# Kernel optimization log

Measured on AMD Instinct MI355X. Metric: run time of the kernel, lower is better.

The kernel has to match this reference:

```python
import jax, jax.numpy as jnp
import numpy as np

B, S, D, H = 4, 2048, 1024, 16
HD = D // H  # head_dim = 64


def setup_inputs() -> dict:
    key = jax.random.key(0)
    ks = jax.random.split(key, 11)
    scale = 1.0 / np.sqrt(D)
    return {
        "query": jax.random.normal(ks[0], (B, S, D), jnp.float32),
        "key": jax.random.normal(ks[1], (B, S, D), jnp.float32),
        "value": jax.random.normal(ks[2], (B, S, D), jnp.float32),
        "Wq": jax.random.normal(ks[3], (D, D), jnp.float32) * scale,
        "bq": jnp.zeros((D,), jnp.float32),
        "Wk": jax.random.normal(ks[4], (D, D), jnp.float32) * scale,
        "bk": jnp.zeros((D,), jnp.float32),
        "Wv": jax.random.normal(ks[5], (D, D), jnp.float32) * scale,
        "bv": jnp.zeros((D,), jnp.float32),
        "Wo": jax.random.normal(ks[6], (D, D), jnp.float32) * scale,
        "bo": jnp.zeros((D,), jnp.float32),
    }


def _split_heads(x):
    # [B, S, D] -> [B, H, S, HD]
    return x.reshape(B, -1, H, HD).transpose(0, 2, 1, 3)


def reference(query, key, value, Wq, bq, Wk, bk, Wv, bv, Wo, bo):
    # QKV projections in fp32, then cast to fp16 (faithful to the torch code)
    q = (query @ Wq.T + bq).astype(jnp.float16)
    k = (key @ Wk.T + bk).astype(jnp.float16)
    v = (value @ Wv.T + bv).astype(jnp.float16)
    q, k, v = _split_heads(q), _split_heads(k), _split_heads(v)
    # scores in fp16, scaled by sqrt(head_dim)
    energy = jnp.einsum("bhqd,bhkd->bhqk", q, k) / jnp.float16(np.sqrt(HD))
    attention = jax.nn.softmax(energy, axis=-1)  # fp16 softmax, as in torch
    x = jnp.einsum("bhqk,bhkd->bhqd", attention, v).astype(jnp.float32)
    x = x.transpose(0, 2, 1, 3).reshape(B, -1, D)  # merge heads
    return x @ Wo.T + bo
```

## Files before the change

### kernel.cpp

```cpp
#include <hip/hip_runtime.h>
#include <cstdint>

#define BB 4
#define SS 2048
#define DD 1024
#define HH 16
#define HDIM 64
#define MTOT (BB*SS)

using half_t = _Float16;
typedef _Float16 half2v __attribute__((ext_vector_type(2)));
typedef _Float16 half4v __attribute__((ext_vector_type(4)));
typedef _Float16 half8v __attribute__((ext_vector_type(8)));
typedef float f32x4 __attribute__((ext_vector_type(4)));

#if defined(__has_builtin)
#if __has_builtin(__builtin_amdgcn_exp2f)
#define ATTN_EXP2(x) __builtin_amdgcn_exp2f(x)
#endif
#if __has_builtin(__builtin_amdgcn_cvt_pkrtz)
#define ATTN_PKRTZ 1
#endif
#endif

__device__ __forceinline__ void glds16(const half_t* g, half_t* l) {
    __builtin_amdgcn_global_load_lds(g, l, 16, 0, 0);
}

__global__ __launch_bounds__(256) void split_hi_lo(const float* __restrict__ x,
    half_t* __restrict__ hi, half_t* __restrict__ lo, int n4)
{
    const int i = blockIdx.x * blockDim.x + threadIdx.x;
    if (i >= n4) return;
    float4 v = reinterpret_cast<const float4*>(x)[i];
    float vv[4] = {v.x, v.y, v.z, v.w};
    half4v h, l;
    #pragma unroll
    for (int j = 0; j < 4; ++j) {
        half_t hh = (half_t)vv[j];
        h[j] = hh;
        l[j] = (half_t)(vv[j] - (float)hh);
    }
    reinterpret_cast<half4v*>(hi)[i] = h;
    reinterpret_cast<half4v*>(lo)[i] = l;
}

__global__ __launch_bounds__(256) void cast_w4(
    const float* __restrict__ w0, const float* __restrict__ w1,
    const float* __restrict__ w2, const float* __restrict__ w3,
    half_t* __restrict__ hi)
{
    const int z = blockIdx.z;
    const float* src = z == 0 ? w0 : z == 1 ? w1 : z == 2 ? w2 : w3;
    const size_t base4 = (size_t)z * (DD * DD / 4);
    const size_t i = base4 + blockIdx.x * 256 + threadIdx.x;
    float4 v = reinterpret_cast<const float4*>(src)[blockIdx.x * 256 + threadIdx.x];
    float vv[4] = {v.x, v.y, v.z, v.w};
    half4v h;
    #pragma unroll
    for (int j = 0; j < 4; ++j) h[j] = (half_t)vv[j];
    reinterpret_cast<half4v*>(hi)[i] = h;
}

__global__ __launch_bounds__(256, 4) void gemm_proj(
    const float* __restrict__ A0, const float* __restrict__ A1,
    const float* __restrict__ A2,
    const half_t* __restrict__ WH,
    const float* __restrict__ B0, const float* __restrict__ B1,
    const float* __restrict__ B2,
    half_t* __restrict__ C0, half_t* __restrict__ C1, half_t* __restrict__ C2)
{
    __shared__ __align__(16) half_t AhS[2][128 * 32];
    __shared__ __align__(16) half_t WhS[2][128 * 32];

    const int z = blockIdx.z;
    const float*  A    = z == 0 ? A0 : z == 1 ? A1 : A2;
    const float*  bias = z == 0 ? B0 : z == 1 ? B1 : B2;
    half_t*       C    = z == 0 ? C0 : z == 1 ? C1 : C2;
    const half_t* WHz  = WH + (size_t)z * (DD * DD);

    const int tid = threadIdx.x;
    const int l = tid & 63, w = tid >> 6;
    const int lr = l & 15, lg = l >> 4;
    const int wr = w >> 1, wc = w & 1;
    const int m0 = blockIdx.x * 128, n0 = blockIdx.y * 128;

    const int arow = tid >> 2;
    const int acol = (tid & 3) * 8;
    const int wlrow = l >> 2, wlcol = (l & 3) * 8;

    f32x4 acc[4][4] = {};
    float4 av[2][2];

    #pragma unroll
    for (int j = 0; j < 2; ++j) {
        const float* ap = A + (size_t)(m0 + j * 64 + arow) * DD + acol;
        av[j][0] = *reinterpret_cast<const float4*>(ap);
        av[j][1] = *reinterpret_cast<const float4*>(ap + 4);
    }
    #pragma unroll
    for (int j = 0; j < 2; ++j) {
        half_t hb[8];
        float v0[4] = {av[j][0].x, av[j][0].y, av[j][0].z, av[j][0].w};
        float v1[4] = {av[j][1].x, av[j][1].y, av[j][1].z, av[j][1].w};
        #pragma unroll
        for (int e = 0; e < 4; ++e) { hb[e] = (half_t)v0[e]; hb[4 + e] = (half_t)v1[e]; }
        *reinterpret_cast<int4*>(&AhS[0][(j * 64 + arow) * 32 + acol]) = *reinterpret_cast<int4*>(hb);
    }
    #pragma unroll
    for (int i = 0; i < 2; ++i) {
        const int rr = (w * 2 + i) * 16 + wlrow;
        glds16(WHz + (size_t)(n0 + rr) * DD + wlcol, &WhS[0][(w * 2 + i) * 512]);
    }
    #pragma unroll
    for (int j = 0; j < 2; ++j) {
        const float* ap = A + (size_t)(m0 + j * 64 + arow) * DD + 32 + acol;
        av[j][0] = *reinterpret_cast<const float4*>(ap);
        av[j][1] = *reinterpret_cast<const float4*>(ap + 4);
    }
    __syncthreads();

    for (int t = 0; t < 32; ++t) {
        const int cur = t & 1, nxt = cur ^ 1;
        if (t < 31) {
            const int kk1 = (t + 1) * 32;
            #pragma unroll
            for (int i = 0; i < 2; ++i) {
                const int rr = (w * 2 + i) * 16 + wlrow;
                glds16(WHz + (size_t)(n0 + rr) * DD + kk1 + wlcol, &WhS[nxt][(w * 2 + i) * 512]);
            }
            #pragma unroll
            for (int j = 0; j < 2; ++j) {
                half_t hb[8];
                float v0[4] = {av[j][0].x, av[j][0].y, av[j][0].z, av[j][0].w};
                float v1[4] = {av[j][1].x, av[j][1].y, av[j][1].z, av[j][1].w};
                #pragma unroll
                for (int e = 0; e < 4; ++e) { hb[e] = (half_t)v0[e]; hb[4 + e] = (half_t)v1[e]; }
                *reinterpret_cast<int4*>(&AhS[nxt][(j * 64 + arow) * 32 + acol]) = *reinterpret_cast<int4*>(hb);
            }
        }

        half8v af[4];
        #pragma unroll
        for (int mt = 0; mt < 4; ++mt)
            af[mt] = *reinterpret_cast<const half8v*>(&AhS[cur][(wr * 64 + mt * 16 + lr) * 32 + 8 * lg]);
        #pragma unroll
        for (int nt = 0; nt < 4; ++nt) {
            half8v wf = *reinterpret_cast<const half8v*>(&WhS[cur][(wc * 64 + nt * 16 + lr) * 32 + 8 * lg]);
            #pragma unroll
            for (int mt = 0; mt < 4; ++mt)
                acc[mt][nt] = __builtin_amdgcn_mfma_f32_16x16x32_f16(af[mt], wf, acc[mt][nt], 0, 0, 0);
        }

        if (t < 30) {
            const int kk2 = (t + 2) * 32;
            #pragma unroll
            for (int j = 0; j < 2; ++j) {
                const float* ap = A + (size_t)(m0 + j * 64 + arow) * DD + kk2 + acol;
                av[j][0] = *reinterpret_cast<const float4*>(ap);
                av[j][1] = *reinterpret_cast<const float4*>(ap + 4);
            }
        }
        __syncthreads();
    }

    #pragma unroll
    for (int nt = 0; nt < 4; ++nt) {
        const int n = n0 + wc * 64 + nt * 16 + lr;
        const float bn = bias[n];
        #pragma unroll
        for (int mt = 0; mt < 4; ++mt) {
            const int mbase = m0 + wr * 64 + mt * 16 + 4 * lg;
            #pragma unroll
            for (int j = 0; j < 4; ++j)
                C[(size_t)(mbase + j) * DD + n] = (half_t)(acc[mt][nt][j] + bn);
        }
    }
}

__global__ __launch_bounds__(256, 4) void gemm_out(
    const half_t* __restrict__ Ag,
    const half_t* __restrict__ WHz,
    const float* __restrict__ bias, float* __restrict__ C)
{
    __shared__ __align__(16) half_t AhS[2][128 * 32];
    __shared__ __align__(16) half_t WhS[2][128 * 32];

    const int tid = threadIdx.x;
    const int l = tid & 63, w = tid >> 6;
    const int lr = l & 15, lg = l >> 4;
    const int wr = w >> 1, wc = w & 1;
    const int m0 = blockIdx.x * 128, n0 = blockIdx.y * 128;
    const int wlrow = l >> 2, wlcol = (l & 3) * 8;

    f32x4 acc[4][4] = {};

    #pragma unroll
    for (int i = 0; i < 2; ++i) {
        const int rr = (w * 2 + i) * 16 + wlrow;
        glds16(Ag  + (size_t)(m0 + rr) * DD + wlcol, &AhS[0][(w * 2 + i) * 512]);
        glds16(WHz + (size_t)(n0 + rr) * DD + wlcol, &WhS[0][(w * 2 + i) * 512]);
    }
    __syncthreads();

    for (int t = 0; t < 32; ++t) {
        const int cur = t & 1, nxt = cur ^ 1;
        if (t < 31) {
            const int kk1 = (t + 1) * 32;
            #pragma unroll
            for (int i = 0; i < 2; ++i) {
                const int rr = (w * 2 + i) * 16 + wlrow;
                glds16(Ag  + (size_t)(m0 + rr) * DD + kk1 + wlcol, &AhS[nxt][(w * 2 + i) * 512]);
                glds16(WHz + (size_t)(n0 + rr) * DD + kk1 + wlcol, &WhS[nxt][(w * 2 + i) * 512]);
            }
        }

        half8v af[4];
        #pragma unroll
        for (int mt = 0; mt < 4; ++mt)
            af[mt] = *reinterpret_cast<const half8v*>(&AhS[cur][(wr * 64 + mt * 16 + lr) * 32 + 8 * lg]);
        #pragma unroll
        for (int nt = 0; nt < 4; ++nt) {
            half8v wf = *reinterpret_cast<const half8v*>(&WhS[cur][(wc * 64 + nt * 16 + lr) * 32 + 8 * lg]);
            #pragma unroll
            for (int mt = 0; mt < 4; ++mt)
                acc[mt][nt] = __builtin_amdgcn_mfma_f32_16x16x32_f16(af[mt], wf, acc[mt][nt], 0, 0, 0);
        }
        __syncthreads();
    }

    #pragma unroll
    for (int nt = 0; nt < 4; ++nt) {
        const int n = n0 + wc * 64 + nt * 16 + lr;
        const float bn = bias[n];
        #pragma unroll
        for (int mt = 0; mt < 4; ++mt) {
            const int mbase = m0 + wr * 64 + mt * 16 + 4 * lg;
            #pragma unroll
            for (int j = 0; j < 4; ++j)
                C[(size_t)(mbase + j) * DD + n] = acc[mt][nt][j] + bn;
        }
    }
}

template<int MODE, typename TC>
__global__ __launch_bounds__(256) void gemm3s(
    const half_t* __restrict__ Ah, const half_t* __restrict__ Al,
    const float* __restrict__ Af,
    const half_t* __restrict__ Wh, const half_t* __restrict__ Wl,
    const float* __restrict__ bias, TC* __restrict__ C,
    int Kdim, int Ndim)
{
    constexpr int LDT = 72;
    __shared__ __align__(16) half_t As[128 * LDT];
    __shared__ __align__(16) half_t Ws[128 * LDT];
    const int tid = threadIdx.x;
    const int l = tid & 63, w = tid >> 6;
    const int lr = l & 15, lg = l >> 4;
    const int wr = w >> 1, wc = w & 1;
    const int m0 = blockIdx.y * 128, n0 = blockIdx.x * 128;
    const int r = tid >> 1, t = tid & 1;

    f32x4 acc[4][4] = {};

    for (int kk = 0; kk < Kdim; kk += 32) {
        __syncthreads();
        if constexpr (MODE == 1) {
            const float* ap = Af + (size_t)(m0 + r) * Kdim + kk + 16 * t;
            half_t hbuf[16], lbuf[16];
            #pragma unroll
            for (int u = 0; u < 4; ++u) {
                float4 v = *reinterpret_cast<const float4*>(ap + 4 * u);
                float vv[4] = {v.x, v.y, v.z, v.w};
                #pragma unroll
                for (int j = 0; j < 4; ++j) {
                    half_t hh = (half_t)vv[j];
                    hbuf[4 * u + j] = hh;
                    lbuf[4 * u + j] = (half_t)(vv[j] - (float)hh);
                }
            }
            *reinterpret_cast<int4*>(&As[r * LDT + 16 * t])          = *reinterpret_cast<int4*>(hbuf);
            *reinterpret_cast<int4*>(&As[r * LDT + 16 * t + 8])      = *reinterpret_cast<int4*>(hbuf + 8);
            *reinterpret_cast<int4*>(&As[r * LDT + 40 + 16 * t])     = *reinterpret_cast<int4*>(lbuf);
            *reinterpret_cast<int4*>(&As[r * LDT + 40 + 16 * t + 8]) = *reinterpret_cast<int4*>(lbuf + 8);
        } else {
            const half_t* ap = Ah + (size_t)(m0 + r) * Kdim + kk + 16 * t;
            *reinterpret_cast<int4*>(&As[r * LDT + 16 * t])     = *reinterpret_cast<const int4*>(ap);
            *reinterpret_cast<int4*>(&As[r * LDT + 16 * t + 8]) = *reinterpret_cast<const int4*>(ap + 8);
        }
        {
            const half_t* wp = Wh + (size_t)(n0 + r) * Kdim + kk + 16 * t;
            *reinterpret_cast<int4*>(&Ws[r * LDT + 16 * t])     = *reinterpret_cast<const int4*>(wp);
            *reinterpret_cast<int4*>(&Ws[r * LDT + 16 * t + 8]) = *reinterpret_cast<const int4*>(wp + 8);
            const half_t* wlp = Wl + (size_t)(n0 + r) * Kdim + kk + 16 * t;
            *reinterpret_cast<int4*>(&Ws[r * LDT + 40 + 16 * t])     = *reinterpret_cast<const int4*>(wlp);
            *reinterpret_cast<int4*>(&Ws[r * LDT + 40 + 16 * t + 8]) = *reinterpret_cast<const int4*>(wlp + 8);
        }
        __syncthreads();

        half8v af[4], alf[4];
        #pragma unroll
        for (int mt = 0; mt < 4; ++mt) {
            af[mt] = *reinterpret_cast<const half8v*>(&As[(wr * 64 + mt * 16 + lr) * LDT + 8 * lg]);
            if constexpr (MODE != 2)
                alf[mt] = *reinterpret_cast<const half8v*>(&As[(wr * 64 + mt * 16 + lr) * LDT + 40 + 8 * lg]);
        }
        #pragma unroll
        for (int nt = 0; nt < 4; ++nt) {
            half8v wf  = *reinterpret_cast<const half8v*>(&Ws[(wc * 64 + nt * 16 + lr) * LDT + 8 * lg]);
            half8v wlf = *reinterpret_cast<const half8v*>(&Ws[(wc * 64 + nt * 16 + lr) * LDT + 40 + 8 * lg]);
            #pragma unroll
            for (int mt = 0; mt < 4; ++mt) {
                acc[mt][nt] = __builtin_amdgcn_mfma_f32_16x16x32_f16(af[mt], wf, acc[mt][nt], 0, 0, 0);
                acc[mt][nt] = __builtin_amdgcn_mfma_f32_16x16x32_f16(af[mt], wlf, acc[mt][nt], 0, 0, 0);
                if constexpr (MODE != 2)
                    acc[mt][nt] = __builtin_amdgcn_mfma_f32_16x16x32_f16(alf[mt], wf, acc[mt][nt], 0, 0, 0);
            }
        }
    }

    #pragma unroll
    for (int nt = 0; nt < 4; ++nt) {
        const int n = n0 + wc * 64 + nt * 16 + lr;
        const float bn = bias[n];
        #pragma unroll
        for (int mt = 0; mt < 4; ++mt) {
            const int mbase = m0 + wr * 64 + mt * 16 + 4 * lg;
            #pragma unroll
            for (int j = 0; j < 4; ++j) {
                float v = acc[mt][nt][j] + bn;
                if constexpr (sizeof(TC) == 4)
                    C[(size_t)(mbase + j) * Ndim + n] = v;
                else
                    C[(size_t)(mbase + j) * Ndim + n] = (half_t)v;
            }
        }
    }
}

template<typename TA, typename TC>
__global__ __launch_bounds__(256) void gemm_bias(const TA* __restrict__ A,
    const float* __restrict__ W, const float* __restrict__ bias,
    TC* __restrict__ C, int Mdim, int Ndim, int Kdim)
{
    constexpr int BK = 16;
    __shared__ float As[BK][68];
    __shared__ float Ws[BK][68];
    const int tx = threadIdx.x, ty = threadIdx.y;
    const int tid = ty * 16 + tx;
    const int m0 = blockIdx.y * 64, n0 = blockIdx.x * 64;
    const int lrow = tid >> 2;
    const int lc4  = (tid & 3) * 4;

    float acc[4][4] = {};
    for (int kk = 0; kk < Kdim; kk += BK) {
        {
            const TA* ap = A + (size_t)(m0 + lrow) * Kdim + kk + lc4;
            float a0, a1, a2, a3;
            if constexpr (sizeof(TA) == 4) {
                float4 v = *reinterpret_cast<const float4*>(ap);
                a0 = v.x; a1 = v.y; a2 = v.z; a3 = v.w;
            } else {
                half2v v0 = *reinterpret_cast<const half2v*>(ap);
                half2v v1 = *reinterpret_cast<const half2v*>(ap + 2);
                a0 = (float)v0[0]; a1 = (float)v0[1];
                a2 = (float)v1[0]; a3 = (float)v1[1];
            }
            As[lc4 + 0][lrow] = a0; As[lc4 + 1][lrow] = a1;
            As[lc4 + 2][lrow] = a2; As[lc4 + 3][lrow] = a3;
            const float* wp = W + (size_t)(n0 + lrow) * Kdim + kk + lc4;
            float4 wv = *reinterpret_cast<const float4*>(wp);
            Ws[lc4 + 0][lrow] = wv.x; Ws[lc4 + 1][lrow] = wv.y;
            Ws[lc4 + 2][lrow] = wv.z; Ws[lc4 + 3][lrow] = wv.w;
        }
        __syncthreads();
        #pragma unroll
        for (int k = 0; k < BK; ++k) {
            float4 av = *reinterpret_cast<const float4*>(&As[k][ty * 4]);
            float4 bv = *reinterpret_cast<const float4*>(&Ws[k][tx * 4]);
            float a[4] = {av.x, av.y, av.z, av.w};
            float b[4] = {bv.x, bv.y, bv.z, bv.w};
            #pragma unroll
            for (int i = 0; i < 4; ++i)
                #pragma unroll
                for (int j = 0; j < 4; ++j)
                    acc[i][j] = fmaf(a[i], b[j], acc[i][j]);
        }
        __syncthreads();
    }
    #pragma unroll
    for (int i = 0; i < 4; ++i) {
        const int m = m0 + ty * 4 + i;
        #pragma unroll
        for (int j = 0; j < 4; ++j) {
            const int n = n0 + tx * 4 + j;
            float v = acc[i][j] + bias[n];
            if constexpr (sizeof(TC) == 4)
                C[(size_t)m * Ndim + n] = v;
            else
                C[(size_t)m * Ndim + n] = (half_t)v;
        }
    }
}

__global__ __launch_bounds__(256, 4) void attn_fused(const half_t* __restrict__ Q,
    const half_t* __restrict__ K, const half_t* __restrict__ V,
    half_t* __restrict__ X)
{
    __shared__ __align__(16) half_t KsL[2][64 * 64];
    __shared__ __align__(16) half_t Vt[2][64 * 72];

    const int tid = threadIdx.x;
    const int l   = tid & 63;
    const int w   = tid >> 6;
    const int lr  = l & 15;
    const int lg  = l >> 4;

    const int phys = blockIdx.x;
    const int virt = (phys & 7) * 128 + (phys >> 3);
    const int qb = virt & 15;
    const int h  = (virt >> 4) & 15;
    const int b  = virt >> 8;

    const int q0 = qb * 128 + w * 32;
    const size_t hoff = (size_t)(b * SS) * DD + h * HDIM;

    half8v qf[2][2];
    #pragma unroll
    for (int s = 0; s < 2; ++s) {
        const half_t* qp = Q + hoff + (size_t)(q0 + s * 16 + lr) * DD;
        #pragma unroll
        for (int hb = 0; hb < 2; ++hb) {
            half8v v = *reinterpret_cast<const half8v*>(qp + hb * 32 + 8 * lg);
            #pragma unroll
            for (int e = 0; e < 8; ++e) v[e] *= (half_t)0.125f;
            qf[s][hb] = v;
        }
    }

    int koffH[2];
    #pragma unroll
    for (int i = 0; i < 2; ++i) {
        const int row = (w * 2 + i) * 8 + (l >> 3);
        const int gc  = (l & 7) ^ (row & 7);
        koffH[i] = row * DD + gc * 8;
    }
    const int kidx0 = lr * 64 + ((lg ^ (lr & 7)) * 8);
    const int kidx1 = lr * 64 + (((4 + lg) ^ (lr & 7)) * 8);

    const int vk2 = tid & 31, vdq = tid >> 5;

    float m[2]    = {-1e30f, -1e30f};
    float lsum[2] = {0.f, 0.f};
    f32x4 xacc[2][4] = {};

    half4v va0, va1, vb0, vb1;
    {
        const half_t* kbase = K + hoff;
        glds16(kbase + koffH[0], &KsL[0][(w * 2 + 0) * 512]);
        glds16(kbase + koffH[1], &KsL[0][(w * 2 + 1) * 512]);
        const half_t* vsrc = V + hoff + (size_t)(2 * vk2) * DD + vdq * 8;
        va0 = *reinterpret_cast<const half4v*>(vsrc);
        va1 = *reinterpret_cast<const half4v*>(vsrc + 4);
        vb0 = *reinterpret_cast<const half4v*>(vsrc + DD);
        vb1 = *reinterpret_cast<const half4v*>(vsrc + DD + 4);
        #pragma unroll
        for (int i = 0; i < 4; ++i) {
            half2v p0 = {va0[i], vb0[i]};
            half2v p1 = {va1[i], vb1[i]};
            *reinterpret_cast<half2v*>(&Vt[0][(vdq * 8 + i) * 72 + 2 * vk2])     = p0;
            *reinterpret_cast<half2v*>(&Vt[0][(vdq * 8 + i + 4) * 72 + 2 * vk2]) = p1;
        }
    }
    __syncthreads();

    for (int t = 0; t < SS / 64; ++t) {
        const int cur = t & 1, nxt = cur ^ 1;
        if (t < SS / 64 - 1) {
            const half_t* kbase = K + hoff + (size_t)(t + 1) * 64 * DD;
            glds16(kbase + koffH[0], &KsL[nxt][(w * 2 + 0) * 512]);
            glds16(kbase + koffH[1], &KsL[nxt][(w * 2 + 1) * 512]);
            const half_t* vsrc = V + hoff + (size_t)((t + 1) * 64 + 2 * vk2) * DD + vdq * 8;
            va0 = *reinterpret_cast<const half4v*>(vsrc);
            va1 = *reinterpret_cast<const half4v*>(vsrc + 4);
            vb0 = *reinterpret_cast<const half4v*>(vsrc + DD);
            vb1 = *reinterpret_cast<const half4v*>(vsrc + DD + 4);
        }

        half8v kf[4][2];
        #pragma unroll
        for (int kb = 0; kb < 4; ++kb) {
            kf[kb][0] = *reinterpret_cast<const half8v*>(&KsL[cur][kb * 1024 + kidx0]);
            kf[kb][1] = *reinterpret_cast<const half8v*>(&KsL[cur][kb * 1024 + kidx1]);
        }

        half4v af[2][4];
        #pragma unroll
        for (int s = 0; s < 2; ++s) {
            f32x4 c[4] = {};
            __builtin_amdgcn_s_setprio(1);
            #pragma unroll
            for (int kb = 0; kb < 4; ++kb)
                #pragma unroll
                for (int hb = 0; hb < 2; ++hb)
                    c[kb] = __builtin_amdgcn_mfma_f32_16x16x32_f16(kf[kb][hb], qf[s][hb], c[kb], 0, 0, 0);
            __builtin_amdgcn_s_setprio(0);

            float r0 = fmaxf(fmaxf(c[0][0], c[0][1]), fmaxf(c[0][2], c[0][3]));
            float r1 = fmaxf(fmaxf(c[1][0], c[1][1]), fmaxf(c[1][2], c[1][3]));
            float r2 = fmaxf(fmaxf(c[2][0], c[2][1]), fmaxf(c[2][2], c[2][3]));
            float r3 = fmaxf(fmaxf(c[3][0], c[3][1]), fmaxf(c[3][2], c[3][3]));
            float rmax = fmaxf(fmaxf(r0, r1), fmaxf(r2, r3));
            rmax = fmaxf(rmax, __shfl_xor(rmax, 16, 64));
            rmax = fmaxf(rmax, __shfl_xor(rmax, 32, 64));

            if (__any(rmax > m[s] + 8.0f)) {
                const float mn = fmaxf(m[s], rmax);
                const float sc = __expf(m[s] - mn);
                lsum[s] *= sc;
                #pragma unroll
                for (int db = 0; db < 4; ++db)
                    #pragma unroll
                    for (int j = 0; j < 4; ++j)
                        xacc[s][db][j] *= sc;
                m[s] = mn;
            }

            const float L2E = 1.4426950408889634f;
            const float nm2 = m[s] * -L2E;
            float ps = 0.f;
            #pragma unroll
            for (int kb = 0; kb < 4; ++kb) {
#ifdef ATTN_EXP2
                const float p0 = ATTN_EXP2(__builtin_fmaf(c[kb][0], L2E, nm2));
                const float p1 = ATTN_EXP2(__builtin_fmaf(c[kb][1], L2E, nm2));
                const float p2 = ATTN_EXP2(__builtin_fmaf(c[kb][2], L2E, nm2));
                const float p3 = ATTN_EXP2(__builtin_fmaf(c[kb][3], L2E, nm2));
#else
                const float p0 = __expf(c[kb][0] - m[s]);
                const float p1 = __expf(c[kb][1] - m[s]);
                const float p2 = __expf(c[kb][2] - m[s]);
                const float p3 = __expf(c[kb][3] - m[s]);
#endif
                ps += (p0 + p1) + (p2 + p3);
#ifdef ATTN_PKRTZ
                auto lo = __builtin_amdgcn_cvt_pkrtz(p0, p1);
                auto hi = __builtin_amdgcn_cvt_pkrtz(p2, p3);
                af[s][kb][0] = (half_t)lo[0]; af[s][kb][1] = (half_t)lo[1];
                af[s][kb][2] = (half_t)hi[0]; af[s][kb][3] = (half_t)hi[1];
#else
                af[s][kb][0] = (half_t)p0; af[s][kb][1] = (half_t)p1;
                af[s][kb][2] = (half_t)p2; af[s][kb][3] = (half_t)p3;
#endif
            }
            ps += __shfl_xor(ps, 16, 64);
            ps += __shfl_xor(ps, 32, 64);
            lsum[s] += ps;
        }

        __builtin_amdgcn_s_setprio(1);
        #pragma unroll
        for (int db = 0; db < 4; ++db)
            #pragma unroll
            for (int kb = 0; kb < 4; ++kb) {
                half4v vf = *reinterpret_cast<const half4v*>(
                    &Vt[cur][(db * 16 + lr) * 72 + kb * 16 + 4 * lg]);
                xacc[0][db] = __builtin_amdgcn_mfma_f32_16x16x16f16(vf, af[0][kb], xacc[0][db], 0, 0, 0);
                xacc[1][db] = __builtin_amdgcn_mfma_f32_16x16x16f16(vf, af[1][kb], xacc[1][db], 0, 0, 0);
            }
        __builtin_amdgcn_s_setprio(0);

        if (t < SS / 64 - 1) {
            #pragma unroll
            for (int i = 0; i < 4; ++i) {
                half2v p0 = {va0[i], vb0[i]};
                half2v p1 = {va1[i], vb1[i]};
                *reinterpret_cast<half2v*>(&Vt[nxt][(vdq * 8 + i) * 72 + 2 * vk2])     = p0;
                *reinterpret_cast<half2v*>(&Vt[nxt][(vdq * 8 + i + 4) * 72 + 2 * vk2]) = p1;
            }
        }
        __syncthreads();
    }

    #pragma unroll
    for (int s = 0; s < 2; ++s) {
        const float invl = 1.0f / lsum[s];
        half_t* xp = X + hoff + (size_t)(q0 + s * 16 + lr) * DD;
        #pragma unroll
        for (int db = 0; db < 4; ++db) {
            half4v o;
            #pragma unroll
            for (int j = 0; j < 4; ++j) o[j] = (half_t)(xacc[s][db][j] * invl);
            *reinterpret_cast<half4v*>(xp + db * 16 + 4 * lg) = o;
        }
    }
}

extern "C" void kernel_launch(void* const* d_in, const int* in_sizes, int n_in,
                              void* d_out, int out_size, void* d_ws, size_t ws_size,
                              hipStream_t stream) {
    const float* q   = (const float*)d_in[0];
    const float* k   = (const float*)d_in[1];
    const float* v   = (const float*)d_in[2];
    const float* Wq  = (const float*)d_in[3];
    const float* bq  = (const float*)d_in[4];
    const float* Wk  = (const float*)d_in[5];
    const float* bk  = (const float*)d_in[6];
    const float* Wv  = (const float*)d_in[7];
    const float* bv  = (const float*)d_in[8];
    const float* Wo  = (const float*)d_in[9];
    const float* bo  = (const float*)d_in[10];
    float* out = (float*)d_out;

    const size_t MB = 1ull << 20;
    const size_t ACT = (size_t)MTOT * DD;
    const size_t WEL = (size_t)DD * DD;

    half_t* q16 = (half_t*)d_ws;
    half_t* k16 = q16 + ACT;
    half_t* v16 = k16 + ACT;
    half_t* x16 = v16 + ACT;

    dim3 gblk(256);
    dim3 ablk(256);
    dim3 agrd(1024);

    if (ws_size >= 76 * MB) {
        half_t* wh = x16 + ACT;

        dim3 wsgrd(WEL / 4 / 256, 1, 4);
        hipLaunchKernelGGL(cast_w4, wsgrd, gblk, 0, stream,
                           Wq, Wk, Wv, Wo, wh);

        dim3 pgrd(MTOT / 128, DD / 128, 3);
        hipLaunchKernelGGL(gemm_proj, pgrd, gblk, 0, stream,
                           q, k, v, wh, bq, bk, bv, q16, k16, v16);

        hipLaunchKernelGGL(attn_fused, agrd, ablk, 0, stream, q16, k16, v16, x16);

        dim3 ogrd(MTOT / 128, DD / 128);
        hipLaunchKernelGGL(gemm_out, ogrd, gblk, 0, stream,
                           x16, wh + 3 * WEL, bo, out);
    } else if (ws_size >= 72 * MB) {
        half_t* wh = x16 + ACT;
        half_t* wl = wh + WEL;
        const int nw4 = (int)(WEL / 4);
        dim3 sgW((nw4 + 255) / 256);
        dim3 ggrd(DD / 128, MTOT / 128);

        hipLaunchKernelGGL(split_hi_lo, sgW, gblk, 0, stream, Wq, wh, wl, nw4);
        hipLaunchKernelGGL((gemm3s<1, half_t>), ggrd, gblk, 0, stream,
                           nullptr, nullptr, q, wh, wl, bq, q16, DD, DD);
        hipLaunchKernelGGL(split_hi_lo, sgW, gblk, 0, stream, Wk, wh, wl, nw4);
        hipLaunchKernelGGL((gemm3s<1, half_t>), ggrd, gblk, 0, stream,
                           nullptr, nullptr, k, wh, wl, bk, k16, DD, DD);
        hipLaunchKernelGGL(split_hi_lo, sgW, gblk, 0, stream, Wv, wh, wl, nw4);
        hipLaunchKernelGGL((gemm3s<1, half_t>), ggrd, gblk, 0, stream,
                           nullptr, nullptr, v, wh, wl, bv, v16, DD, DD);

        hipLaunchKernelGGL(attn_fused, agrd, ablk, 0, stream, q16, k16, v16, x16);

        hipLaunchKernelGGL(split_hi_lo, sgW, gblk, 0, stream, Wo, wh, wl, nw4);
        hipLaunchKernelGGL((gemm3s<2, float>), ggrd, gblk, 0, stream,
                           x16, nullptr, nullptr, wh, wl, bo, out, DD, DD);
    } else {
        dim3 blk(16, 16);
        dim3 grd(DD / 64, MTOT / 64);
        hipLaunchKernelGGL((gemm_bias<float, half_t>), grd, blk, 0, stream,
                           q, Wq, bq, q16, MTOT, DD, DD);
        hipLaunchKernelGGL((gemm_bias<float, half_t>), grd, blk, 0, stream,
                           k, Wk, bk, k16, MTOT, DD, DD);
        hipLaunchKernelGGL((gemm_bias<float, half_t>), grd, blk, 0, stream,
                           v, Wv, bv, v16, MTOT, DD, DD);
        hipLaunchKernelGGL(attn_fused, agrd, ablk, 0, stream, q16, k16, v16, x16);
        hipLaunchKernelGGL((gemm_bias<half_t, float>), grd, blk, 0, stream,
                           x16, Wo, bo, out, MTOT, DD, DD);
    }
}
```

Baseline: 221.7 us.

## Use 16x16x32 MFMA for PV product via permuted K-row staging

Switches the P·V matmul from 16x16x16 MFMAs to 16x16x32 MFMAs, halving the instruction count and using 8-wide LDS reads of V. To make the probability fragments from the QK^T accumulators line up with the wider K dimension, K rows are loaded into shared memory in a permuted order, so the score columns come out in the order the new MFMA expects. The permutation has to match the V layout exactly, otherwise results will be wrong.

```diff
diff --git a/kernel.cpp b/kernel.cpp
--- a/kernel.cpp
+++ b/kernel.cpp
@@ -441,9 +441,11 @@
     int koffH[2];
     #pragma unroll
     for (int i = 0; i < 2; ++i) {
-        const int row = (w * 2 + i) * 8 + (l >> 3);
-        const int gc  = (l & 7) ^ (row & 7);
-        koffH[i] = row * DD + gc * 8;
+        const int R    = (w * 2 + i) * 8 + (l >> 3);
+        const int gkey = ((R >> 5) & 1) * 32 + ((R >> 2) & 3) * 8
+                       + ((R >> 4) & 1) * 4 + (R & 3);
+        const int gc   = (l & 7) ^ (R & 7);
+        koffH[i] = gkey * DD + gc * 8;
     }
     const int kidx0 = lr * 64 + ((lg ^ (lr & 7)) * 8);
     const int kidx1 = lr * 64 + (((4 + lg) ^ (lr & 7)) * 8);
@@ -494,7 +496,7 @@
             kf[kb][1] = *reinterpret_cast<const half8v*>(&KsL[cur][kb * 1024 + kidx1]);
         }
 
-        half4v af[2][4];
+        half8v af2[2][2];
         #pragma unroll
         for (int s = 0; s < 2; ++s) {
             f32x4 c[4] = {};
@@ -546,11 +548,15 @@
 #ifdef ATTN_PKRTZ
                 auto lo = __builtin_amdgcn_cvt_pkrtz(p0, p1);
                 auto hi = __builtin_amdgcn_cvt_pkrtz(p2, p3);
-                af[s][kb][0] = (half_t)lo[0]; af[s][kb][1] = (half_t)lo[1];
-                af[s][kb][2] = (half_t)hi[0]; af[s][kb][3] = (half_t)hi[1];
+                af2[s][kb >> 1][(kb & 1) * 4 + 0] = (half_t)lo[0];
+                af2[s][kb >> 1][(kb & 1) * 4 + 1] = (half_t)lo[1];
+                af2[s][kb >> 1][(kb & 1) * 4 + 2] = (half_t)hi[0];
+                af2[s][kb >> 1][(kb & 1) * 4 + 3] = (half_t)hi[1];
 #else
-                af[s][kb][0] = (half_t)p0; af[s][kb][1] = (half_t)p1;
-                af[s][kb][2] = (half_t)p2; af[s][kb][3] = (half_t)p3;
+                af2[s][kb >> 1][(kb & 1) * 4 + 0] = (half_t)p0;
+                af2[s][kb >> 1][(kb & 1) * 4 + 1] = (half_t)p1;
+                af2[s][kb >> 1][(kb & 1) * 4 + 2] = (half_t)p2;
+                af2[s][kb >> 1][(kb & 1) * 4 + 3] = (half_t)p3;
 #endif
             }
             ps += __shfl_xor(ps, 16, 64);
@@ -562,11 +568,11 @@
         #pragma unroll
         for (int db = 0; db < 4; ++db)
             #pragma unroll
-            for (int kb = 0; kb < 4; ++kb) {
-                half4v vf = *reinterpret_cast<const half4v*>(
-                    &Vt[cur][(db * 16 + lr) * 72 + kb * 16 + 4 * lg]);
-                xacc[0][db] = __builtin_amdgcn_mfma_f32_16x16x16f16(vf, af[0][kb], xacc[0][db], 0, 0, 0);
-                xacc[1][db] = __builtin_amdgcn_mfma_f32_16x16x16f16(vf, af[1][kb], xacc[1][db], 0, 0, 0);
+            for (int kb2 = 0; kb2 < 2; ++kb2) {
+                half8v vf = *reinterpret_cast<const half8v*>(
+                    &Vt[cur][(db * 16 + lr) * 72 + kb2 * 32 + 8 * lg]);
+                xacc[0][db] = __builtin_amdgcn_mfma_f32_16x16x32_f16(vf, af2[0][kb2], xacc[0][db], 0, 0, 0);
+                xacc[1][db] = __builtin_amdgcn_mfma_f32_16x16x32_f16(vf, af2[1][kb2], xacc[1][db], 0, 0, 0);
             }
         __builtin_amdgcn_s_setprio(0);
 
```

New measurement: 211.9 us, median of 2. 1.05x faster.
